# Optimization experiments

Hardware: AMD Instinct MI355X
Metric: run time of the kernel (lower is better)

The kernel has to match this reference:

```python
import jax, jax.numpy as jnp
import numpy as np

C_IN = 256
C_INTER = 128  # in_channels // reduction
B, H, W = 8, 64, 64


def setup_inputs() -> dict:
    key = jax.random.key(0)
    ks = jax.random.split(key, 9)
    s_in = 1.0 / np.sqrt(C_IN)
    s_int = 1.0 / np.sqrt(C_INTER)
    return {
        "x": jax.random.normal(ks[0], (B, C_IN, H, W), dtype=jnp.float32),
        "Wg": jax.random.uniform(ks[1], (C_INTER, C_IN), jnp.float32, -s_in, s_in),
        "bg": jax.random.uniform(ks[2], (C_INTER,), jnp.float32, -s_in, s_in),
        "Wt": jax.random.uniform(ks[3], (C_INTER, C_IN), jnp.float32, -s_in, s_in),
        "bt": jax.random.uniform(ks[4], (C_INTER,), jnp.float32, -s_in, s_in),
        "Wp": jax.random.uniform(ks[5], (C_INTER, C_IN), jnp.float32, -s_in, s_in),
        "bp": jax.random.uniform(ks[6], (C_INTER,), jnp.float32, -s_in, s_in),
        "Wo": jax.random.uniform(ks[7], (C_IN, C_INTER), jnp.float32, -s_int, s_int),
        "bo": jax.random.uniform(ks[8], (C_IN,), jnp.float32, -s_int, s_int),
    }


def reference(x, Wg, bg, Wt, bt, Wp, bp, Wo, bo):
    n, C, h, w = x.shape
    xf = x.reshape(n, C, h * w)                      # [n, C, L]
    # 1x1 convs == per-pixel linear projections
    g = jnp.einsum('dc,ncl->nld', Wg, xf) + bg       # [n, L, ci]
    th = jnp.einsum('dc,ncl->nld', Wt, xf) + bt      # [n, L, ci]
    ph = jnp.einsum('dc,ncl->ndl', Wp, xf) + bp[:, None]  # [n, ci, L]
    # embedded gaussian attention: softmax(theta @ phi) @ g
    scores = jnp.einsum('nld,ndm->nlm', th, ph)      # [n, L, L]
    attn = jax.nn.softmax(scores, axis=-1)
    y = jnp.einsum('nlm,nmd->nld', attn, g)          # [n, L, ci]
    out = jnp.einsum('cd,nld->ncl', Wo, y) + bo[None, :, None]  # [n, C, L]
    return out.reshape(n, C, h, w) + x
```

## Files before the change

### kernel.cpp

```cpp
#include <hip/hip_runtime.h>
#include <hip/hip_bf16.h>

#define NB  8
#define CIN 256
#define CI  128
#define LPX 4096

typedef __attribute__((ext_vector_type(8))) short short8;
typedef __attribute__((ext_vector_type(4))) float f32x4;

#define MFMA(a,b,c) __builtin_amdgcn_mfma_f32_16x16x32_bf16((a),(b),(c),0,0,0)

__global__ __launch_bounds__(256) void cvt_kernel(
    const float* __restrict__ Wt, const float* __restrict__ Wp,
    const float* __restrict__ Wg, const float* __restrict__ Wo,
    __hip_bfloat16* __restrict__ WB, __hip_bfloat16* __restrict__ WoB)
{
  int idx = blockIdx.x * 256 + threadIdx.x;
  for (int i = idx; i < 384 * 256 + 256 * 128; i += 256 * 256) {
    if (i < 384 * 256) {
      float v = (i < 32768) ? Wt[i] : (i < 65536) ? Wp[i - 32768] : Wg[i - 65536];
      WB[i] = __float2bfloat16(v);
    } else {
      int j = i - 384 * 256;
      WoB[j] = __float2bfloat16(Wo[j]);
    }
  }
}

__global__ __launch_bounds__(256) void proj_kernel(
    const float* __restrict__ x,
    const __hip_bfloat16* __restrict__ WB,
    const float* __restrict__ bt, const float* __restrict__ bp,
    const float* __restrict__ bg,
    __hip_bfloat16* __restrict__ Q, __hip_bfloat16* __restrict__ Kv,
    __hip_bfloat16* __restrict__ VT)
{
  alignas(16) __shared__ __hip_bfloat16 xT[64][264];
  alignas(16) __shared__ __hip_bfloat16 vst[64][136];
  const int bid = blockIdx.x;
  const int n = bid >> 6, lt = bid & 63, l0 = lt * 64;
  const int t = threadIdx.x;

  const float* xn = x + (size_t)n * CIN * LPX;
  for (int idx = t; idx < CIN * 64; idx += 256) {
    int c = idx >> 6, l = idx & 63;
    xT[l][c] = __float2bfloat16(xn[(size_t)c * LPX + l0 + l]);
  }
  __syncthreads();

  const int w = t >> 6, lane = t & 63, fr = lane & 15, fq = lane >> 4;

  short8 af[8];
#pragma unroll
  for (int ks = 0; ks < 8; ++ks)
    af[ks] = *(const short8*)&xT[w * 16 + fr][ks * 32 + fq * 8];

  for (int dt = 0; dt < 24; ++dt) {
    int dl = (dt & 7) * 16 + fr;
    float bb = (dt < 8) ? bt[dl] : (dt < 16) ? bp[dl] : bg[dl];
    f32x4 acc = { bb, bb, bb, bb };
#pragma unroll
    for (int ks = 0; ks < 8; ++ks) {
      short8 bf = *(const short8*)&WB[(size_t)(dt * 16 + fr) * CIN + ks * 32 + fq * 8];
      acc = MFMA(af[ks], bf, acc);
    }
    if (dt < 16) {
      __hip_bfloat16* dst = (dt < 8) ? Q : Kv;
#pragma unroll
      for (int r = 0; r < 4; ++r) {
        int l = l0 + w * 16 + fq * 4 + r;
        dst[((size_t)n * LPX + l) * CI + dl] = __float2bfloat16(acc[r]);
      }
    } else {
#pragma unroll
      for (int r = 0; r < 4; ++r)
        vst[w * 16 + fq * 4 + r][dl] = __float2bfloat16(acc[r]);
    }
  }
  __syncthreads();
#pragma unroll
  for (int iter = 0; iter < 32; ++iter) {
    int dv = (t >> 6) * 32 + iter;
    int lc = t & 63;
    VT[((size_t)n * CI + dv) * LPX + l0 + lc] = vst[lc][dv];
  }
}

__global__ __launch_bounds__(256) void attn_kernel(
    const __hip_bfloat16* __restrict__ Q, const __hip_bfloat16* __restrict__ Kv,
    const __hip_bfloat16* __restrict__ VT, const __hip_bfloat16* __restrict__ WoB,
    const float* __restrict__ bo, const float* __restrict__ x,
    float* __restrict__ out)
{
  union ShU {
    struct { __hip_bfloat16 Kl[64][136]; __hip_bfloat16 Vl[128][72]; } kv;
    __hip_bfloat16 yl[64][136];
  };
  alignas(16) __shared__ ShU sh;
  alignas(16) __shared__ __hip_bfloat16 Pl[4][16][72];

  const int bid = blockIdx.x;
  const int n = bid >> 6, qt = bid & 63, l0 = qt * 64;
  const int t = threadIdx.x;
  const int w = t >> 6, lane = t & 63, fr = lane & 15, fq = lane >> 4;

  const __hip_bfloat16* Qn = Q  + (size_t)n * LPX * CI;
  const __hip_bfloat16* Kn = Kv + (size_t)n * LPX * CI;
  const __hip_bfloat16* Vn = VT + (size_t)n * CI * LPX;

  short8 qf[4];
  const int ql = l0 + w * 16 + fr;
#pragma unroll
  for (int ks = 0; ks < 4; ++ks)
    qf[ks] = *(const short8*)&Qn[(size_t)ql * CI + ks * 32 + fq * 8];

  f32x4 yacc[8];
#pragma unroll
  for (int dt = 0; dt < 8; ++dt) yacc[dt] = f32x4{0.f, 0.f, 0.f, 0.f};
  float run_l[4] = {0.f, 0.f, 0.f, 0.f};

  const int krow = t >> 2, kseg = t & 3;
  const int vrow = t >> 1, vseg = t & 1;

  for (int m0 = 0; m0 < LPX; m0 += 64) {
    __syncthreads();
    {
      const uint4* sk = (const uint4*)&Kn[(size_t)(m0 + krow) * CI + kseg * 32];
      uint4 k0 = sk[0], k1 = sk[1], k2 = sk[2], k3 = sk[3];
      const uint4* sv = (const uint4*)&Vn[(size_t)vrow * LPX + m0 + vseg * 32];
      uint4 v0 = sv[0], v1 = sv[1], v2 = sv[2], v3 = sv[3];
      *(uint4*)&sh.kv.Kl[krow][kseg * 32]      = k0;
      *(uint4*)&sh.kv.Kl[krow][kseg * 32 + 8]  = k1;
      *(uint4*)&sh.kv.Kl[krow][kseg * 32 + 16] = k2;
      *(uint4*)&sh.kv.Kl[krow][kseg * 32 + 24] = k3;
      *(uint4*)&sh.kv.Vl[vrow][vseg * 32]      = v0;
      *(uint4*)&sh.kv.Vl[vrow][vseg * 32 + 8]  = v1;
      *(uint4*)&sh.kv.Vl[vrow][vseg * 32 + 16] = v2;
      *(uint4*)&sh.kv.Vl[vrow][vseg * 32 + 24] = v3;
    }
    __syncthreads();

    f32x4 s[4];
#pragma unroll
    for (int mt = 0; mt < 4; ++mt) s[mt] = f32x4{0.f, 0.f, 0.f, 0.f};
#pragma unroll
    for (int ks = 0; ks < 4; ++ks) {
#pragma unroll
      for (int mt = 0; mt < 4; ++mt) {
        short8 kf = *(const short8*)&sh.kv.Kl[mt * 16 + fr][ks * 32 + fq * 8];
        s[mt] = MFMA(qf[ks], kf, s[mt]);
      }
    }

#pragma unroll
    for (int r = 0; r < 4; ++r) {
      float p0 = __expf(s[0][r]);
      float p1 = __expf(s[1][r]);
      float p2 = __expf(s[2][r]);
      float p3 = __expf(s[3][r]);
      run_l[r] += (p0 + p1) + (p2 + p3);
      Pl[w][fq * 4 + r][fr]      = __float2bfloat16(p0);
      Pl[w][fq * 4 + r][16 + fr] = __float2bfloat16(p1);
      Pl[w][fq * 4 + r][32 + fr] = __float2bfloat16(p2);
      Pl[w][fq * 4 + r][48 + fr] = __float2bfloat16(p3);
    }

#pragma unroll
    for (int ks = 0; ks < 2; ++ks) {
      short8 pf = *(const short8*)&Pl[w][fr][ks * 32 + fq * 8];
#pragma unroll
      for (int dt = 0; dt < 8; ++dt) {
        short8 vf = *(const short8*)&sh.kv.Vl[dt * 16 + fr][ks * 32 + fq * 8];
        yacc[dt] = MFMA(pf, vf, yacc[dt]);
      }
    }
  }

  __syncthreads();

  float inv[4];
#pragma unroll
  for (int r = 0; r < 4; ++r) {
    float rs = run_l[r];
#pragma unroll
    for (int off = 1; off < 16; off <<= 1)
      rs += __shfl_xor(rs, off);
    inv[r] = 1.0f / rs;
  }
#pragma unroll
  for (int dt = 0; dt < 8; ++dt)
#pragma unroll
    for (int r = 0; r < 4; ++r)
      sh.yl[w * 16 + fq * 4 + r][dt * 16 + fr] = __float2bfloat16(yacc[dt][r] * inv[r]);
  __syncthreads();

  for (int ct = 0; ct < 16; ++ct) {
    f32x4 o = f32x4{0.f, 0.f, 0.f, 0.f};
#pragma unroll
    for (int ks = 0; ks < 4; ++ks) {
      short8 wf = *(const short8*)&WoB[(size_t)(ct * 16 + fr) * CI + ks * 32 + fq * 8];
      short8 yf = *(const short8*)&sh.yl[w * 16 + fr][ks * 32 + fq * 8];
      o = MFMA(wf, yf, o);
    }
#pragma unroll
    for (int r = 0; r < 4; ++r) {
      int c = ct * 16 + fq * 4 + r;
      size_t gi = ((size_t)n * CIN + c) * LPX + l0 + w * 16 + fr;
      out[gi] = o[r] + bo[c] + x[gi];
    }
  }
}

extern "C" void kernel_launch(void* const* d_in, const int* in_sizes, int n_in,
                              void* d_out, int out_size, void* d_ws, size_t ws_size,
                              hipStream_t stream) {
  const float* x  = (const float*)d_in[0];
  const float* Wg = (const float*)d_in[1];
  const float* bg = (const float*)d_in[2];
  const float* Wt = (const float*)d_in[3];
  const float* bt = (const float*)d_in[4];
  const float* Wp = (const float*)d_in[5];
  const float* bp = (const float*)d_in[6];
  const float* Wo = (const float*)d_in[7];
  const float* bo = (const float*)d_in[8];
  float* out = (float*)d_out;

  char* ws = (char*)d_ws;
  const size_t SZ = (size_t)NB * LPX * CI * 2;
  __hip_bfloat16* Q   = (__hip_bfloat16*)(ws);
  __hip_bfloat16* Kv  = (__hip_bfloat16*)(ws + SZ);
  __hip_bfloat16* VT  = (__hip_bfloat16*)(ws + 2 * SZ);
  __hip_bfloat16* WB  = (__hip_bfloat16*)(ws + 3 * SZ);
  __hip_bfloat16* WoB = (__hip_bfloat16*)(ws + 3 * SZ + 384 * 256 * 2);

  cvt_kernel<<<256, 256, 0, stream>>>(Wt, Wp, Wg, Wo, WB, WoB);
  proj_kernel<<<512, 256, 0, stream>>>(x, WB, bt, bp, bg, Q, Kv, VT);
  attn_kernel<<<512, 256, 0, stream>>>(Q, Kv, VT, WoB, bo, x, out);
}
```

Before: 305.0 us.

## Restructure attention loop with 32x32 MFMA, register P exchange, and double-buffered KV

The attention kernel now uses 32x32x16 MFMAs and computes S transposed, so the exp'd probabilities can be repacked into the PV operand with cross-lane shuffles instead of a shared-memory round trip. The four waves split 2x2 over query rows and key columns, and partial y results are combined through shared memory at the end. K/V tiles are double-buffered, with the next tile's global loads issued before compute, and the loop drops to one barrier per iteration. The cost is more registers (launch bounds of 2 blocks per CU), doubled LDS for the KV buffers, and a final cross-wave reduction.

```diff
diff --git a/kernel.cpp b/kernel.cpp
--- a/kernel.cpp
+++ b/kernel.cpp
@@ -8,8 +8,23 @@
 
 typedef __attribute__((ext_vector_type(8))) short short8;
 typedef __attribute__((ext_vector_type(4))) float f32x4;
-
-#define MFMA(a,b,c) __builtin_amdgcn_mfma_f32_16x16x32_bf16((a),(b),(c),0,0,0)
+typedef __attribute__((ext_vector_type(16))) float f32x16;
+
+#define MFMA16(a,b,c) __builtin_amdgcn_mfma_f32_16x16x32_bf16((a),(b),(c),0,0,0)
+#define MFMA32(a,b,c) __builtin_amdgcn_mfma_f32_32x32x16_bf16((a),(b),(c),0,0,0)
+
+__device__ __forceinline__ unsigned cvtpk_bf16(float lo, float hi) {
+  unsigned r;
+  asm("v_cvt_pk_bf16_f32 %0, %1, %2" : "=v"(r) : "v"(lo), "v"(hi));
+  return r;
+}
+
+__device__ __forceinline__ f32x16 zero16() {
+  f32x16 v;
+#pragma unroll
+  for (int i = 0; i < 16; ++i) v[i] = 0.f;
+  return v;
+}
 
 __global__ __launch_bounds__(256) void cvt_kernel(
     const float* __restrict__ Wt, const float* __restrict__ Wp,
@@ -63,7 +78,7 @@
 #pragma unroll
     for (int ks = 0; ks < 8; ++ks) {
       short8 bf = *(const short8*)&WB[(size_t)(dt * 16 + fr) * CIN + ks * 32 + fq * 8];
-      acc = MFMA(af[ks], bf, acc);
+      acc = MFMA16(af[ks], bf, acc);
     }
     if (dt < 16) {
       __hip_bfloat16* dst = (dt < 8) ? Q : Kv;
@@ -87,121 +102,150 @@
   }
 }
 
-__global__ __launch_bounds__(256) void attn_kernel(
+struct KVBuf {
+  __hip_bfloat16 Kl[64][136];
+  __hip_bfloat16 Vl[128][72];
+};
+
+__global__ __launch_bounds__(256, 2) void attn_kernel(
     const __hip_bfloat16* __restrict__ Q, const __hip_bfloat16* __restrict__ Kv,
     const __hip_bfloat16* __restrict__ VT, const __hip_bfloat16* __restrict__ WoB,
     const float* __restrict__ bo, const float* __restrict__ x,
     float* __restrict__ out)
 {
-  union ShU {
-    struct { __hip_bfloat16 Kl[64][136]; __hip_bfloat16 Vl[128][72]; } kv;
-    __hip_bfloat16 yl[64][136];
-  };
-  alignas(16) __shared__ ShU sh;
-  alignas(16) __shared__ __hip_bfloat16 Pl[4][16][72];
+  alignas(16) __shared__ KVBuf bufs[2];
+  __shared__ float rbuf[2][2][32];
 
   const int bid = blockIdx.x;
   const int n = bid >> 6, qt = bid & 63, l0 = qt * 64;
   const int t = threadIdx.x;
-  const int w = t >> 6, lane = t & 63, fr = lane & 15, fq = lane >> 4;
+  const int w = t >> 6, lane = t & 63;
+  const int l5 = lane & 31, hi = lane >> 5;
+  const int wq = w >> 1, wm = w & 1;
 
   const __hip_bfloat16* Qn = Q  + (size_t)n * LPX * CI;
   const __hip_bfloat16* Kn = Kv + (size_t)n * LPX * CI;
   const __hip_bfloat16* Vn = VT + (size_t)n * CI * LPX;
 
-  short8 qf[4];
-  const int ql = l0 + w * 16 + fr;
-#pragma unroll
-  for (int ks = 0; ks < 4; ++ks)
-    qf[ks] = *(const short8*)&Qn[(size_t)ql * CI + ks * 32 + fq * 8];
-
-  f32x4 yacc[8];
-#pragma unroll
-  for (int dt = 0; dt < 8; ++dt) yacc[dt] = f32x4{0.f, 0.f, 0.f, 0.f};
-  float run_l[4] = {0.f, 0.f, 0.f, 0.f};
+  short8 qa[8];
+#pragma unroll
+  for (int ks = 0; ks < 8; ++ks)
+    qa[ks] = *(const short8*)&Qn[(size_t)(l0 + wq * 32 + l5) * CI + ks * 16 + hi * 8];
+
+  f32x16 yacc[4];
+#pragma unroll
+  for (int d = 0; d < 4; ++d) yacc[d] = zero16();
+  float runl = 0.f;
 
   const int krow = t >> 2, kseg = t & 3;
   const int vrow = t >> 1, vseg = t & 1;
-
-  for (int m0 = 0; m0 < LPX; m0 += 64) {
+  uint4 kr[4], vr[4];
+
+#define LOADKV(M0) do {                                                        \
+    const uint4* sk_ = (const uint4*)&Kn[(size_t)((M0) + krow) * CI + kseg*32];\
+    kr[0]=sk_[0]; kr[1]=sk_[1]; kr[2]=sk_[2]; kr[3]=sk_[3];                    \
+    const uint4* sv_ = (const uint4*)&Vn[(size_t)vrow * LPX + (M0) + vseg*32]; \
+    vr[0]=sv_[0]; vr[1]=sv_[1]; vr[2]=sv_[2]; vr[3]=sv_[3];                    \
+  } while(0)
+
+#define WRITEKV(B) do {                                                        \
+    *(uint4*)&(B)->Kl[krow][kseg*32]      = kr[0];                             \
+    *(uint4*)&(B)->Kl[krow][kseg*32 + 8]  = kr[1];                             \
+    *(uint4*)&(B)->Kl[krow][kseg*32 + 16] = kr[2];                             \
+    *(uint4*)&(B)->Kl[krow][kseg*32 + 24] = kr[3];                             \
+    *(uint4*)&(B)->Vl[vrow][vseg*32]      = vr[0];                             \
+    *(uint4*)&(B)->Vl[vrow][vseg*32 + 8]  = vr[1];                             \
+    *(uint4*)&(B)->Vl[vrow][vseg*32 + 16] = vr[2];                             \
+    *(uint4*)&(B)->Vl[vrow][vseg*32 + 24] = vr[3];                             \
+  } while(0)
+
+  LOADKV(0);
+  WRITEKV(&bufs[0]);
+
+  for (int it = 0; it < 64; ++it) {
     __syncthreads();
-    {
-      const uint4* sk = (const uint4*)&Kn[(size_t)(m0 + krow) * CI + kseg * 32];
-      uint4 k0 = sk[0], k1 = sk[1], k2 = sk[2], k3 = sk[3];
-      const uint4* sv = (const uint4*)&Vn[(size_t)vrow * LPX + m0 + vseg * 32];
-      uint4 v0 = sv[0], v1 = sv[1], v2 = sv[2], v3 = sv[3];
-      *(uint4*)&sh.kv.Kl[krow][kseg * 32]      = k0;
-      *(uint4*)&sh.kv.Kl[krow][kseg * 32 + 8]  = k1;
-      *(uint4*)&sh.kv.Kl[krow][kseg * 32 + 16] = k2;
-      *(uint4*)&sh.kv.Kl[krow][kseg * 32 + 24] = k3;
-      *(uint4*)&sh.kv.Vl[vrow][vseg * 32]      = v0;
-      *(uint4*)&sh.kv.Vl[vrow][vseg * 32 + 8]  = v1;
-      *(uint4*)&sh.kv.Vl[vrow][vseg * 32 + 16] = v2;
-      *(uint4*)&sh.kv.Vl[vrow][vseg * 32 + 24] = v3;
-    }
-    __syncthreads();
-
-    f32x4 s[4];
-#pragma unroll
-    for (int mt = 0; mt < 4; ++mt) s[mt] = f32x4{0.f, 0.f, 0.f, 0.f};
-#pragma unroll
-    for (int ks = 0; ks < 4; ++ks) {
-#pragma unroll
-      for (int mt = 0; mt < 4; ++mt) {
-        short8 kf = *(const short8*)&sh.kv.Kl[mt * 16 + fr][ks * 32 + fq * 8];
-        s[mt] = MFMA(qf[ks], kf, s[mt]);
-      }
-    }
-
-#pragma unroll
-    for (int r = 0; r < 4; ++r) {
-      float p0 = __expf(s[0][r]);
-      float p1 = __expf(s[1][r]);
-      float p2 = __expf(s[2][r]);
-      float p3 = __expf(s[3][r]);
-      run_l[r] += (p0 + p1) + (p2 + p3);
-      Pl[w][fq * 4 + r][fr]      = __float2bfloat16(p0);
-      Pl[w][fq * 4 + r][16 + fr] = __float2bfloat16(p1);
-      Pl[w][fq * 4 + r][32 + fr] = __float2bfloat16(p2);
-      Pl[w][fq * 4 + r][48 + fr] = __float2bfloat16(p3);
-    }
-
-#pragma unroll
-    for (int ks = 0; ks < 2; ++ks) {
-      short8 pf = *(const short8*)&Pl[w][fr][ks * 32 + fq * 8];
-#pragma unroll
-      for (int dt = 0; dt < 8; ++dt) {
-        short8 vf = *(const short8*)&sh.kv.Vl[dt * 16 + fr][ks * 32 + fq * 8];
-        yacc[dt] = MFMA(pf, vf, yacc[dt]);
-      }
-    }
-  }
-
-  __syncthreads();
-
-  float inv[4];
-#pragma unroll
-  for (int r = 0; r < 4; ++r) {
-    float rs = run_l[r];
-#pragma unroll
-    for (int off = 1; off < 16; off <<= 1)
-      rs += __shfl_xor(rs, off);
-    inv[r] = 1.0f / rs;
-  }
-#pragma unroll
-  for (int dt = 0; dt < 8; ++dt)
-#pragma unroll
-    for (int r = 0; r < 4; ++r)
-      sh.yl[w * 16 + fq * 4 + r][dt * 16 + fr] = __float2bfloat16(yacc[dt][r] * inv[r]);
-  __syncthreads();
-
+    KVBuf* cb = &bufs[it & 1];
+    if (it < 63) LOADKV((it + 1) * 64);
+
+    f32x16 sT = zero16();
+#pragma unroll
+    for (int ks = 0; ks < 8; ++ks) {
+      short8 kf = *(const short8*)&cb->Kl[wm * 32 + l5][ks * 16 + hi * 8];
+      sT = MFMA32(kf, qa[ks], sT);
+    }
+
+    float p[16];
+#pragma unroll
+    for (int r = 0; r < 16; ++r) { p[r] = __expf(sT[r]); runl += p[r]; }
+
+#pragma unroll
+    for (int mstep = 0; mstep < 2; ++mstep) {
+      const int g = mstep * 8;
+      unsigned a0 = cvtpk_bf16(p[g + 0], p[g + 1]);
+      unsigned a1 = cvtpk_bf16(p[g + 2], p[g + 3]);
+      unsigned b0 = cvtpk_bf16(p[g + 4], p[g + 5]);
+      unsigned b1 = cvtpk_bf16(p[g + 6], p[g + 7]);
+      unsigned sa0 = (unsigned)__shfl_xor((int)a0, 32);
+      unsigned sa1 = (unsigned)__shfl_xor((int)a1, 32);
+      unsigned sb0 = (unsigned)__shfl_xor((int)b0, 32);
+      unsigned sb1 = (unsigned)__shfl_xor((int)b1, 32);
+      union { unsigned u[4]; short8 s; } pk;
+      pk.u[0] = hi ? sb0 : a0;
+      pk.u[1] = hi ? sb1 : a1;
+      pk.u[2] = hi ? b0  : sa0;
+      pk.u[3] = hi ? b1  : sa1;
+#pragma unroll
+      for (int dblk = 0; dblk < 4; ++dblk) {
+        short8 vf = *(const short8*)&cb->Vl[dblk * 32 + l5]
+                                         [wm * 32 + mstep * 16 + hi * 8];
+        yacc[dblk] = MFMA32(pk.s, vf, yacc[dblk]);
+      }
+    }
+
+    if (it < 63) WRITEKV(&bufs[(it + 1) & 1]);
+  }
+
+  __syncthreads();
+
+  runl += __shfl_xor(runl, 32);
+  if (lane < 32) rbuf[wm][wq][lane] = runl;
+
+  float* ys = (float*)&bufs[0];
+  if (wm == 1) {
+#pragma unroll
+    for (int dblk = 0; dblk < 4; ++dblk)
+#pragma unroll
+      for (int r = 0; r < 16; ++r) {
+        int row = (r & 3) + 8 * (r >> 2) + 4 * hi;
+        ys[(size_t)(wq * 32 + row) * 128 + dblk * 32 + l5] = yacc[dblk][r];
+      }
+  }
+  __syncthreads();
+
+  __hip_bfloat16* yl = (__hip_bfloat16*)&bufs[1];
+  if (wm == 0) {
+#pragma unroll
+    for (int r = 0; r < 16; ++r) {
+      int row = (r & 3) + 8 * (r >> 2) + 4 * hi;
+      float iv = 1.0f / (rbuf[0][wq][row] + rbuf[1][wq][row]);
+#pragma unroll
+      for (int dblk = 0; dblk < 4; ++dblk) {
+        float v = yacc[dblk][r] +
+                  ys[(size_t)(wq * 32 + row) * 128 + dblk * 32 + l5];
+        yl[(size_t)(wq * 32 + row) * 136 + dblk * 32 + l5] = __float2bfloat16(v * iv);
+      }
+    }
+  }
+  __syncthreads();
+
+  const int fr = lane & 15, fq = lane >> 4;
   for (int ct = 0; ct < 16; ++ct) {
     f32x4 o = f32x4{0.f, 0.f, 0.f, 0.f};
 #pragma unroll
     for (int ks = 0; ks < 4; ++ks) {
       short8 wf = *(const short8*)&WoB[(size_t)(ct * 16 + fr) * CI + ks * 32 + fq * 8];
-      short8 yf = *(const short8*)&sh.yl[w * 16 + fr][ks * 32 + fq * 8];
-      o = MFMA(wf, yf, o);
+      short8 yf = *(const short8*)&yl[(size_t)(w * 16 + fr) * 136 + ks * 32 + fq * 8];
+      o = MFMA16(wf, yf, o);
     }
 #pragma unroll
     for (int r = 0; r < 4; ++r) {
@@ -210,6 +254,8 @@
       out[gi] = o[r] + bo[c] + x[gi];
     }
   }
+#undef LOADKV
+#undef WRITEKV
 }
 
 extern "C" void kernel_launch(void* const* d_in, const int* in_sizes, int n_in,
```

After: 246.5 us. -19.2%, faster.
